# Performance work log

Hardware: AMD Instinct MI355X
Metric: run time of the kernel (lower is better)

The kernel has to match this reference:

```python
import jax, jax.numpy as jnp
import numpy as np
from jax import lax

N_TILES = 2097152  # number of 4x4x1 tiles


def setup_inputs() -> dict:
    key = jax.random.key(0)
    kx, kw = jax.random.split(key)
    x = jax.random.normal(kx, (N_TILES, 4, 4, 1), dtype=jnp.float32)
    # spconv SubMConv2d(1, 1, 3) weight, expressed in HWIO layout for lax conv
    W = jax.random.normal(kw, (3, 3, 1, 1), dtype=jnp.float32)
    return {"x": x, "W": W}


def reference(x, W):
    # SparseConvTensor.from_dense: active sites are exactly the nonzero entries
    # (inactive sites hold zeros, which x already encodes).
    x4 = x.reshape(-1, 4, 4, 1)  # [N, 4, 4, 1] NHWC
    active = (x4 != 0).any(axis=-1, keepdims=True)  # [N, 4, 4, 1] bool
    # Submanifold conv == 'same' dense conv restricted to active output sites,
    # since inactive inputs are zero and outputs are only written at active sites.
    y = lax.conv_general_dilated(
        x4, W,
        window_strides=(1, 1), padding="SAME",
        dimension_numbers=("NHWC", "HWIO", "NHWC"),
    )
    y = jnp.where(active, y, jnp.zeros((), y.dtype))
    # spconv.ToDense returns NCHW, matching the torch module's output layout.
    return jnp.transpose(y, (0, 3, 1, 2))  # [N, 1, 4, 4]
```

## Files before the change

kernel.cpp:

```cpp
#include <hip/hip_runtime.h>


__global__ __launch_bounds__(256) void subm_conv44_kernel(
    const float4* __restrict__ x4, const float* __restrict__ W,
    float4* __restrict__ out4, int n_tiles)
{
    int n = blockIdx.x * blockDim.x + threadIdx.x;
    if (n >= n_tiles) return;

    float w[9];
#pragma unroll
    for (int i = 0; i < 9; ++i) w[i] = W[i];

    float4 r[4];
#pragma unroll
    for (int i = 0; i < 4; ++i) r[i] = x4[(size_t)n * 4 + i];

    float xin[4][4];
#pragma unroll
    for (int i = 0; i < 4; ++i) {
        xin[i][0] = r[i].x; xin[i][1] = r[i].y;
        xin[i][2] = r[i].z; xin[i][3] = r[i].w;
    }

    float y[4][4];
#pragma unroll
    for (int i = 0; i < 4; ++i) {
#pragma unroll
        for (int j = 0; j < 4; ++j) {
            float acc = 0.0f;
#pragma unroll
            for (int ki = 0; ki < 3; ++ki) {
                const int si = i + ki - 1;
                if (si < 0 || si > 3) continue;
#pragma unroll
                for (int kj = 0; kj < 3; ++kj) {
                    const int sj = j + kj - 1;
                    if (sj < 0 || sj > 3) continue;
                    acc = fmaf(xin[si][sj], w[ki * 3 + kj], acc);
                }
            }
            y[i][j] = (xin[i][j] != 0.0f) ? acc : 0.0f;
        }
    }

    float4 o[4];
#pragma unroll
    for (int i = 0; i < 4; ++i) {
        o[i].x = y[i][0]; o[i].y = y[i][1];
        o[i].z = y[i][2]; o[i].w = y[i][3];
    }
#pragma unroll
    for (int i = 0; i < 4; ++i) out4[(size_t)n * 4 + i] = o[i];
}

extern "C" void kernel_launch(void* const* d_in, const int* in_sizes, int n_in,
                              void* d_out, int out_size, void* d_ws, size_t ws_size,
                              hipStream_t stream) {
    const float4* x4 = (const float4*)d_in[0];
    const float*  W  = (const float*)d_in[1];
    float4* out4     = (float4*)d_out;

    const int n_tiles = in_sizes[0] / 16;
    const int block = 256;
    const int grid = (n_tiles + block - 1) / block;

    subm_conv44_kernel<<<grid, block, 0, stream>>>(x4, W, out4, n_tiles);
}
```

Baseline: 240.1 us.

## Map one thread per tile row and exchange neighbor rows via shuffles

Each thread now processes one 4-float row of a tile instead of a whole 4x4 tile, so there are four times as many threads. The rows above and below come from the neighbouring lanes through __shfl_up and __shfl_down, with masking at the tile edges. The aim is fully coalesced float4 accesses, where consecutive lanes touch consecutive 16-byte rows, plus more threads in flight to hide memory latency. In exchange the kernel adds eight cross-lane shuffles per thread and loads the weights redundantly across four times as many threads.

```diff
diff --git a/kernel.cpp b/kernel.cpp
--- a/kernel.cpp
+++ b/kernel.cpp
@@ -1,57 +1,50 @@
 #include <hip/hip_runtime.h>
 
 
-__global__ __launch_bounds__(256) void subm_conv44_kernel(
+__global__ __launch_bounds__(256) void subm_conv44_row_kernel(
     const float4* __restrict__ x4, const float* __restrict__ W,
-    float4* __restrict__ out4, int n_tiles)
+    float4* __restrict__ out4, int n_rows)
 {
-    int n = blockIdx.x * blockDim.x + threadIdx.x;
-    if (n >= n_tiles) return;
+    const int gid = blockIdx.x * blockDim.x + threadIdx.x;
+    if (gid >= n_rows) return;
 
     float w[9];
 #pragma unroll
     for (int i = 0; i < 9; ++i) w[i] = W[i];
 
-    float4 r[4];
+    const int r = gid & 3;
+    const float4 c = x4[gid];
+
+    float4 u, d;
+    u.x = __shfl_up(c.x, 1);  u.y = __shfl_up(c.y, 1);
+    u.z = __shfl_up(c.z, 1);  u.w = __shfl_up(c.w, 1);
+    d.x = __shfl_down(c.x, 1); d.y = __shfl_down(c.y, 1);
+    d.z = __shfl_down(c.z, 1); d.w = __shfl_down(c.w, 1);
+
+    const bool hasU = (r > 0);
+    const bool hasD = (r < 3);
+
+    float up[6] = {0.f, hasU ? u.x : 0.f, hasU ? u.y : 0.f,
+                        hasU ? u.z : 0.f, hasU ? u.w : 0.f, 0.f};
+    float mi[6] = {0.f, c.x, c.y, c.z, c.w, 0.f};
+    float dn[6] = {0.f, hasD ? d.x : 0.f, hasD ? d.y : 0.f,
+                        hasD ? d.z : 0.f, hasD ? d.w : 0.f, 0.f};
+
+    float4 o;
+    float* op = &o.x;
 #pragma unroll
-    for (int i = 0; i < 4; ++i) r[i] = x4[(size_t)n * 4 + i];
-
-    float xin[4][4];
+    for (int j = 0; j < 4; ++j) {
+        float acc = 0.0f;
 #pragma unroll
-    for (int i = 0; i < 4; ++i) {
-        xin[i][0] = r[i].x; xin[i][1] = r[i].y;
-        xin[i][2] = r[i].z; xin[i][3] = r[i].w;
+        for (int k = 0; k < 3; ++k) {
+            acc = fmaf(up[j + k], w[0 * 3 + k], acc);
+            acc = fmaf(mi[j + k], w[1 * 3 + k], acc);
+            acc = fmaf(dn[j + k], w[2 * 3 + k], acc);
+        }
+        op[j] = (mi[j + 1] != 0.0f) ? acc : 0.0f;
     }
 
-    float y[4][4];
-#pragma unroll
-    for (int i = 0; i < 4; ++i) {
-#pragma unroll
-        for (int j = 0; j < 4; ++j) {
-            float acc = 0.0f;
-#pragma unroll
-            for (int ki = 0; ki < 3; ++ki) {
-                const int si = i + ki - 1;
-                if (si < 0 || si > 3) continue;
-#pragma unroll
-                for (int kj = 0; kj < 3; ++kj) {
-                    const int sj = j + kj - 1;
-                    if (sj < 0 || sj > 3) continue;
-                    acc = fmaf(xin[si][sj], w[ki * 3 + kj], acc);
-                }
-            }
-            y[i][j] = (xin[i][j] != 0.0f) ? acc : 0.0f;
-        }
-    }
-
-    float4 o[4];
-#pragma unroll
-    for (int i = 0; i < 4; ++i) {
-        o[i].x = y[i][0]; o[i].y = y[i][1];
-        o[i].z = y[i][2]; o[i].w = y[i][3];
-    }
-#pragma unroll
-    for (int i = 0; i < 4; ++i) out4[(size_t)n * 4 + i] = o[i];
+    out4[gid] = o;
 }
 
 extern "C" void kernel_launch(void* const* d_in, const int* in_sizes, int n_in,
@@ -61,9 +54,9 @@
     const float*  W  = (const float*)d_in[1];
     float4* out4     = (float4*)d_out;
 
-    const int n_tiles = in_sizes[0] / 16;
+    const int n_rows = in_sizes[0] / 4;
     const int block = 256;
-    const int grid = (n_tiles + block - 1) / block;
+    const int grid = (n_rows + block - 1) / block;
 
-    subm_conv44_kernel<<<grid, block, 0, stream>>>(x4, W, out4, n_tiles);
+    subm_conv44_row_kernel<<<grid, block, 0, stream>>>(x4, W, out4, n_rows);
 }
```

Result: faster. 218.5 us (-9.0%).
